# Optimization experiments

Hardware: AMD Instinct MI355X
Metric: run time of the kernel (lower is better)

The kernel has to match this reference:

```python
import jax, jax.numpy as jnp
import numpy as np

MIN_NORM = 1e-15
BALL_EPS = 4e-3  # float32 boundary eps used by the PoincareBall manifold


def _norm(x):
    return jnp.maximum(jnp.linalg.norm(x, axis=-1, keepdims=True), MIN_NORM)


def _artanh(x):
    # clamp like torch Artanh autograd fn (1e-7 margin)
    return jnp.arctanh(jnp.clip(x, -1.0 + 1e-7, 1.0 - 1e-7))


def proj(x, c):
    n = _norm(x)
    maxnorm = (1.0 - BALL_EPS) / jnp.sqrt(c)
    return jnp.where(n > maxnorm, x / n * maxnorm, x)


def expmap0(u, c):
    sc = jnp.sqrt(c)
    n = _norm(u)
    return jnp.tanh(sc * n) * u / (sc * n)


def logmap0(p, c):
    sc = jnp.sqrt(c)
    n = _norm(p)
    return _artanh(sc * n) * p / (sc * n)


def mobius_add(x, y, c):
    x2 = jnp.sum(x * x, axis=-1, keepdims=True)
    y2 = jnp.sum(y * y, axis=-1, keepdims=True)
    xy = jnp.sum(x * y, axis=-1, keepdims=True)
    num = (1.0 + 2.0 * c * xy + c * y2) * x + (1.0 - c * x2) * y
    denom = 1.0 + 2.0 * c * xy + c * c * x2 * y2
    return num / jnp.maximum(denom, MIN_NORM)


def mobius_matvec(m, x, c):
    sc = jnp.sqrt(c)
    xn = _norm(x)
    mx = x @ m.T  # [N, out]
    mxn = _norm(mx)
    res = jnp.tanh(mxn / xn * _artanh(sc * xn)) * mx / (mxn * sc)
    is_zero = jnp.all(mx == 0, axis=-1, keepdims=True)
    return jnp.where(is_zero, jnp.zeros_like(res), res)


def setup_inputs() -> dict:
    key = jax.random.key(0)
    N, D_IN, D_OUT, E = 100000, 128, 128, 1600000
    k1, k2, k3, k4, k5 = jax.random.split(key, 5)
    # points inside the Poincare ball (||x|| ~ 0.34 < 1)
    x = 0.03 * jax.random.normal(k1, (N, D_IN), dtype=jnp.float32)
    # xavier_uniform with gain sqrt(2)
    limit = np.sqrt(2.0) * np.sqrt(6.0 / (D_IN + D_OUT))
    weight = jax.random.uniform(k2, (D_OUT, D_IN), minval=-limit, maxval=limit, dtype=jnp.float32)
    bias = jnp.zeros((D_OUT,), dtype=jnp.float32)
    edge_index = jax.random.randint(k3, (2, E), 0, N, dtype=jnp.int64)
    edge_weight = jax.random.uniform(k4, (E,), dtype=jnp.float32) / 16.0
    return {"x": x, "weight": weight, "bias": bias,
            "edge_index": edge_index, "edge_weight": edge_weight,
            "num_nodes": N}


def reference(x, weight, bias, edge_index, edge_weight, num_nodes):
    c_in = 1.0
    c_out = 1.0
    # --- OriginHypLinear (dropout=0 / eval) ---
    mv = proj(mobius_matvec(weight, x, c_in), c_in)
    hyp_bias = proj(expmap0(bias[None, :], c_in), c_in)  # proj_tan0 is identity
    h = proj(mobius_add(mv, hyp_bias, c_in), c_in)
    # --- OriginHypAgg: logmap0 -> spmm -> expmap0 ---
    xt = logmap0(h, c_in)
    dst, src = edge_index[0], edge_index[1]
    support = jax.ops.segment_sum(edge_weight[:, None] * xt[src], dst,
                                  num_segments=num_nodes)
    h = proj(expmap0(support, c_in), c_in)
    # --- OriginHypAct: relu in tangent space ---
    xt = jax.nn.relu(logmap0(h, c_in))  # proj_tan0 identity
    return proj(expmap0(xt, c_out), c_out)
```

## Files before the change

kernel.cpp:

```cpp
#include <hip/hip_runtime.h>
#include <math.h>

#define D 128
#define MAXNORM 0.996f
#define MINNORM 1e-15f
#define ATCLAMP (1.0f - 1e-7f)

#define CHUNK 2048
#define BSH   7
#define MAXNB 1024
#define SCAP2 5120
#define CAP   4096
#define TCAP  (1 << 20)

typedef unsigned int   u32;
typedef unsigned short u16;

typedef __attribute__((ext_vector_type(8))) _Float16 f16x8;
typedef __attribute__((ext_vector_type(2))) __fp16   h2raw;
typedef __attribute__((ext_vector_type(4))) float f32x4;

__device__ __forceinline__ float wsum(float v) {
#pragma unroll
  for (int m = 32; m; m >>= 1) v += __shfl_xor(v, m);
  return v;
}
__device__ __forceinline__ float rsum16(float v) {
#pragma unroll
  for (int m = 1; m <= 8; m <<= 1) v += __shfl_xor(v, m);
  return v;
}

__device__ __forceinline__ float frcp(float x) { return __builtin_amdgcn_rcpf(x); }

__device__ __forceinline__ float fast_artanh(float x) {
  x = fminf(x, ATCLAMP);
  return 0.5f * __logf((1.0f + x) * frcp(1.0f - x));
}
__device__ __forceinline__ float fast_tanh(float z) {
  float t = __expf(-2.0f * z);
  return (1.0f - t) * frcp(1.0f + t);
}

__device__ __forceinline__ float bflo(u32 u) { return __uint_as_float(u << 16); }
__device__ __forceinline__ float bfhi(u32 u) { return __uint_as_float(u & 0xffff0000u); }
__device__ __forceinline__ float bf2f(u16 h) { return __uint_as_float(((u32)h) << 16); }

union H2U { h2raw h; u32 u; };
__device__ __forceinline__ u32 pkh(float a, float b) {
  H2U c; c.h = __builtin_amdgcn_cvt_pkrtz(a, b); return c.u;
}
union U2H { u32 u; _Float16 h[2]; };
union U4H8 { uint4 u; f16x8 h; };
__device__ __forceinline__ f16x8 as_h8(uint4 v) { U4H8 c; c.u = v; return c.h; }
__device__ __forceinline__ u16 f2h(float f) {
  _Float16 h = (_Float16)f; return *(u16*)&h;
}

__device__ __forceinline__ bool detect_bf16(const u32* p) {
  float lo = fabsf(bflo(p[threadIdx.x & 63]));
  return (bool)__all(lo < 1.0f);
}
__device__ __forceinline__ bool detect_i64(const int* p) {
  return (bool)__all(p[2 * (threadIdx.x & 63) + 1] == 0);
}

template<bool BF>
__device__ __forceinline__ void k1_body(const void* xv, const void* Wv,
                                        const void* bv, u16* xt, int N,
                                        uint4* Wh, int blk, int tbase) {
  const int tid  = threadIdx.x;
  const int lane = tid & 63;
  const int wid  = tid >> 6;
  const int qg   = lane >> 4;
  const int lc   = lane & 15;

  for (int slot = tid; slot < 2048; slot += 256) {
    const int l = slot & 63, frag = slot >> 6;
    const int t = frag >> 2, ks = frag & 3;
    const int j  = (l & 15) + 16 * t;
    const int k0 = 32 * ks + 8 * (l >> 4);
    float f[8];
    if (BF) {
      uint4 v = ((const uint4*)Wv)[j * 16 + (k0 >> 3)];
      f[0] = bflo(v.x); f[1] = bfhi(v.x); f[2] = bflo(v.y); f[3] = bfhi(v.y);
      f[4] = bflo(v.z); f[5] = bfhi(v.z); f[6] = bflo(v.w); f[7] = bfhi(v.w);
    } else {
      const float* Wf = (const float*)Wv;
      float4 f0 = *(const float4*)(Wf + (size_t)j * D + k0);
      float4 f1 = *(const float4*)(Wf + (size_t)j * D + k0 + 4);
      f[0]=f0.x; f[1]=f0.y; f[2]=f0.z; f[3]=f0.w;
      f[4]=f1.x; f[5]=f1.y; f[6]=f1.z; f[7]=f1.w;
    }
    Wh[slot] = make_uint4(pkh(f[0],f[1]), pkh(f[2],f[3]),
                          pkh(f[4],f[5]), pkh(f[6],f[7]));
  }

  float bfr[8];
  float nb2 = 0.f;
#pragma unroll
  for (int t = 0; t < 8; ++t) {
    float v = BF ? bf2f(((const u16*)bv)[lc + 16 * t])
                 : ((const float*)bv)[lc + 16 * t];
    bfr[t] = v; nb2 += v * v;
  }
  nb2 = rsum16(nb2);
  float y2;
  {
    float nb = fmaxf(sqrtf(nb2), MINNORM);
    float s  = fast_tanh(nb) * frcp(nb);
    float n1 = s * nb;
    if (n1 > MAXNORM) s *= MAXNORM * frcp(n1);
#pragma unroll
    for (int t = 0; t < 8; ++t) bfr[t] *= s;
    y2 = s * s * nb2;
  }
  const bool bias_zero = (y2 == 0.0f);

  __syncthreads();

  const int T = (N + 15) >> 4;
  const int tile = tbase + blk * 4 + wid;
  if (tile >= T) return;
  {
    const int rbase = tile * 16;
    int rowA = rbase + lc; if (rowA >= N) rowA = N - 1;
    uint4 Ah[4];
    float xn2 = 0.f;
#pragma unroll
    for (int ks = 0; ks < 4; ++ks) {
      float f[8];
      if (BF) {
        uint4 v = ((const uint4*)((const u16*)xv + (size_t)rowA * D))[4 * ks + qg];
        f[0]=bflo(v.x); f[1]=bfhi(v.x); f[2]=bflo(v.y); f[3]=bfhi(v.y);
        f[4]=bflo(v.z); f[5]=bfhi(v.z); f[6]=bflo(v.w); f[7]=bfhi(v.w);
      } else {
        const float4* xr = (const float4*)((const float*)xv + (size_t)rowA * D);
        float4 f0 = xr[8 * ks + 2 * qg], f1 = xr[8 * ks + 2 * qg + 1];
        f[0]=f0.x; f[1]=f0.y; f[2]=f0.z; f[3]=f0.w;
        f[4]=f1.x; f[5]=f1.y; f[6]=f1.z; f[7]=f1.w;
      }
#pragma unroll
      for (int i = 0; i < 8; ++i) xn2 += f[i] * f[i];
      Ah[ks] = make_uint4(pkh(f[0],f[1]), pkh(f[2],f[3]),
                          pkh(f[4],f[5]), pkh(f[6],f[7]));
    }
    xn2 += __shfl_xor(xn2, 16);
    xn2 += __shfl_xor(xn2, 32);

    f32x4 acc[8];
    const f32x4 zero = {0.f, 0.f, 0.f, 0.f};
#pragma unroll
    for (int t = 0; t < 8; ++t) acc[t] = zero;
#pragma unroll
    for (int ks = 0; ks < 4; ++ks) {
      f16x8 a = as_h8(Ah[ks]);
#pragma unroll
      for (int t = 0; t < 8; ++t) {
        f16x8 bh = as_h8(Wh[(t * 4 + ks) * 64 + lane]);
        acc[t] = __builtin_amdgcn_mfma_f32_16x16x32_f16(a, bh, acc[t], 0, 0, 0);
      }
    }

#pragma unroll
    for (int q = 0; q < 4; ++q) {
      const int row_off = qg * 4 + q;
      const int row = rbase + row_off;
      float xnq = fmaxf(sqrtf(__shfl(xn2, row_off)), MINNORM);
      float s2 = 0.f;
#pragma unroll
      for (int t = 0; t < 8; ++t) { float v = acc[t][q]; s2 += v * v; }
      s2 = rsum16(s2);
      float mxn = fmaxf(sqrtf(s2), MINNORM);
      float r = fast_tanh(mxn * frcp(xnq) * fast_artanh(xnq)) * frcp(mxn);
      float pn = r * mxn;
      if (pn > MAXNORM) { r *= MAXNORM * frcp(pn); pn = MAXNORM; }
      float h[8];
      float hn;
      if (bias_zero) {
#pragma unroll
        for (int t = 0; t < 8; ++t) h[t] = r * acc[t][q];
        hn = pn;
      } else {
        float xy = 0.f;
#pragma unroll
        for (int t = 0; t < 8; ++t) { h[t] = r * acc[t][q]; xy += h[t] * bfr[t]; }
        xy = rsum16(xy);
        float x2 = pn * pn;
        float ca = 1.f + 2.f * xy + y2;
        float cb = 1.f - x2;
        float id = frcp(fmaxf(1.f + 2.f * xy + x2 * y2, MINNORM));
        float s3 = 0.f;
#pragma unroll
        for (int t = 0; t < 8; ++t) { h[t] = (ca * h[t] + cb * bfr[t]) * id; s3 += h[t] * h[t]; }
        hn = fmaxf(sqrtf(rsum16(s3)), MINNORM);
      }
      float ps = (hn > MAXNORM) ? (MAXNORM * frcp(hn)) : 1.f;
      float np = fmaxf(hn * ps, MINNORM);
      float tsc = fast_artanh(np) * frcp(np) * ps;
      if (row < N) {
        uint4 pk;
        pk.x = (u32)f2h(tsc * h[0]) | ((u32)f2h(tsc * h[1]) << 16);
        pk.y = (u32)f2h(tsc * h[2]) | ((u32)f2h(tsc * h[3]) << 16);
        pk.z = (u32)f2h(tsc * h[4]) | ((u32)f2h(tsc * h[5]) << 16);
        pk.w = (u32)f2h(tsc * h[6]) | ((u32)f2h(tsc * h[7]) << 16);
        *(uint4*)(xt + (size_t)row * D + lc * 8) = pk;
      }
    }
  }
}

__device__ __forceinline__ void ksA_body(
    const int* ei, const void* ew, uint2* ebuck, u16* soffs,
    int E, int N, int nb, int chunk, uint4* lds) {
  uint2* recs = (uint2*)lds;
  int*   hist = (int*)(lds + 1024);
  int*   sArr = hist + MAXNB;
  int*   psum = sArr + MAXNB + 1;
  const bool i64 = detect_i64(ei);
  const bool bf  = detect_bf16((const u32*)ew);
  const int tid   = threadIdx.x;
  const int cbase = chunk * CHUNK;

  for (int i = tid; i < MAXNB; i += 256) hist[i] = 0;
  __syncthreads();

  int bkt[8], rank[8]; u32 px[8], wb[8]; bool val[8];
#pragma unroll
  for (int r = 0; r < 8; ++r) {
    const int e = cbase + r * 256 + tid;
    val[r] = false;
    if (e < E) {
      int dst, src;
      if (i64) {
        dst = (int)((const uint2*)ei)[(size_t)e].x;
        src = (int)((const uint2*)ei)[(size_t)E + e].x;
      } else {
        dst = ei[e]; src = ei[(size_t)E + e];
      }
      if ((unsigned)dst < (unsigned)N && (unsigned)src < (unsigned)N) {
        val[r] = true;
        bkt[r] = dst >> BSH;
        px[r]  = (u32)src | ((u32)(dst & ((1 << BSH) - 1)) << 17);
        float w;
        if (bf) w = bf2f(((const u16*)ew)[e]); else w = ((const float*)ew)[e];
        wb[r] = __float_as_uint(w);
        rank[r] = atomicAdd(&hist[bkt[r]], 1);
      }
    }
  }
  __syncthreads();

  const int g0 = tid * 4;
  int loc[4], ts = 0;
#pragma unroll
  for (int i = 0; i < 4; ++i) { loc[i] = ts; ts += hist[g0 + i]; }
  psum[tid] = ts; __syncthreads();
#pragma unroll
  for (int off = 1; off < 256; off <<= 1) {
    int t = (tid >= off) ? psum[tid - off] : 0;
    __syncthreads();
    psum[tid] += t;
    __syncthreads();
  }
  const int excl = psum[tid] - ts;
#pragma unroll
  for (int i = 0; i < 4; ++i) sArr[g0 + i] = excl + loc[i];
  if (tid == 255) sArr[MAXNB] = psum[255];
  __syncthreads();

#pragma unroll
  for (int r = 0; r < 8; ++r) if (val[r])
    recs[sArr[bkt[r]] + rank[r]] = make_uint2(px[r], wb[r]);
  __syncthreads();

  const int vcnt = sArr[MAXNB];
  for (int i = tid; i < vcnt; i += 256) ebuck[(size_t)cbase + i] = recs[i];
  u16* so = soffs + (size_t)chunk * (nb + 1);
  for (int b = tid; b <= nb; b += 256) so[b] = (u16)sArr[b];
}

extern "C" __global__ __launch_bounds__(256)
void OriginHyperbolicGraphConvolution_38628935860614_kernel(
    const void* x, const void* W, const void* b, u16* xt,
    const int* ei, const void* ew, uint2* ebuck, u16* soffs, int* tailcur,
    int N, int E, int nb, int nchunks) {
  __shared__ uint4 Wh[2048];
  if (blockIdx.x == 0 && threadIdx.x == 0) *tailcur = 0;
  if ((int)blockIdx.x < nchunks) {
    ksA_body(ei, ew, ebuck, soffs, E, N, nb, (int)blockIdx.x, Wh);
  } else {
    if (detect_bf16((const u32*)x))
      k1_body<true >(x, W, b, xt, N, Wh, (int)blockIdx.x - nchunks, 0);
    else
      k1_body<false>(x, W, b, xt, N, Wh, (int)blockIdx.x - nchunks, 0);
  }
}

__device__ __forceinline__ void ks3_body(
    const uint2* ebuck, const u16* soffs, uint2* esrt, uint2* offs2,
    int* tailcur, int N, int nb, int nchunks, int b, char* smem) {
  uint2* stage = (uint2*)smem;
  int*   red   = (int*)(smem + 40960);
  int*   hist  = (int*)(smem + 41984);
  int*   sc    = (int*)(smem + 42496);
  int*   cur   = (int*)(smem + 43008);
  int*   lcur  = (int*)(smem + 43520);
  u32*   sbase = (u32*)(smem + 43524);
  const int tid = threadIdx.x;
  const int node0 = b << BSH;

  int myc = 0;
  for (int c = tid; c < nchunks; c += 256) {
    const u16* so = soffs + (size_t)c * (nb + 1) + b;
    myc += (int)so[1] - (int)so[0];
  }
  red[tid] = myc;
  if (tid < 128) hist[tid] = 0;
  if (tid == 0) *lcur = 0;
  __syncthreads();
#pragma unroll
  for (int off = 128; off; off >>= 1) {
    if (tid < off) red[tid] += red[tid + off];
    __syncthreads();
  }
  const int cnt = red[0];
  if (tid == 0)
    *sbase = (cnt <= CAP) ? (u32)((size_t)b * CAP)
                          : (u32)((size_t)nb * CAP + (u32)atomicAdd(tailcur, cnt));
  __syncthreads();
  const u32 base = *sbase;

  const bool fit = (cnt <= SCAP2);
  if (fit) {
    for (int c = tid; c < nchunks; c += 256) {
      const u16* so = soffs + (size_t)c * (nb + 1) + b;
      const int a = so[0], e = so[1];
      if (e > a) {
        const int sb = atomicAdd(lcur, e - a);
        for (int j = a; j < e; ++j) {
          const uint2 r = ebuck[(size_t)c * CHUNK + j];
          stage[sb + (j - a)] = r;
          atomicAdd(&hist[(r.x >> 17) & 127], 1);
        }
      }
    }
  } else {
    for (int c = tid; c < nchunks; c += 256) {
      const u16* so = soffs + (size_t)c * (nb + 1) + b;
      for (int j = so[0]; j < so[1]; ++j)
        atomicAdd(&hist[(ebuck[(size_t)c * CHUNK + j].x >> 17) & 127], 1);
    }
  }
  __syncthreads();

  int v = 0;
  if (tid < 128) { v = hist[tid]; sc[tid] = v; }
  __syncthreads();
#pragma unroll
  for (int off = 1; off < 128; off <<= 1) {
    int t = (tid < 128 && tid >= off) ? sc[tid - off] : 0;
    __syncthreads();
    if (tid < 128) sc[tid] += t;
    __syncthreads();
  }
  if (tid < 128) {
    const int st = sc[tid] - v;
    cur[tid] = st;
    const int node = node0 + tid;
    if (node < N) offs2[node] = make_uint2(base + (u32)st, (u32)v);
  }
  __syncthreads();

  if (fit) {
    for (int i = tid; i < cnt; i += 256) {
      const uint2 r = stage[i];
      const int d = atomicAdd(&cur[(r.x >> 17) & 127], 1);
      esrt[(size_t)base + d] = make_uint2(r.x & 0x1FFFFu, r.y);
    }
  } else {
    for (int c = tid; c < nchunks; c += 256) {
      const u16* so = soffs + (size_t)c * (nb + 1) + b;
      for (int j = so[0]; j < so[1]; ++j) {
        const uint2 r = ebuck[(size_t)c * CHUNK + j];
        const int d = atomicAdd(&cur[(r.x >> 17) & 127], 1);
        esrt[(size_t)base + d] = make_uint2(r.x & 0x1FFFFu, r.y);
      }
    }
  }
}

extern "C" __global__ __launch_bounds__(256) void kB(
    const void* x, const void* W, const void* b, u16* xt,
    const uint2* ebuck, const u16* soffs, uint2* esrt, uint2* offs2,
    int* tailcur, int N, int nb, int nchunks, int tbase) {
  __shared__ uint4 smem[2721];
  if ((int)blockIdx.x < nb) {
    ks3_body(ebuck, soffs, esrt, offs2, tailcur, N, nb, nchunks,
             (int)blockIdx.x, (char*)smem);
  } else {
    if (detect_bf16((const u32*)x))
      k1_body<true >(x, W, b, xt, N, smem, (int)blockIdx.x - nb, tbase);
    else
      k1_body<false>(x, W, b, xt, N, smem, (int)blockIdx.x - nb, tbase);
  }
}

extern "C" __global__ __launch_bounds__(256) void kagg(
    const uint2* offs2, const uint2* esrt, const u16* xt,
    void* out, const void* xdet, int N) {
  const bool bf = detect_bf16((const u32*)xdet);
  const int lane = threadIdx.x & 63;
  const int node = blockIdx.x * 4 + (threadIdx.x >> 6);
  if (node >= N) return;
  const uint2 oo = offs2[node];
  const int s0  = __builtin_amdgcn_readfirstlane((int)oo.x);
  const int cnt = __builtin_amdgcn_readfirstlane((int)oo.y);
  const uint2* ep = esrt + s0;
  const u32* xtw = (const u32*)xt;
  float a0 = 0.f, a1 = 0.f;
  int i = 0;
  for (; i + 16 <= cnt; i += 16) {
    uint2 e[16]; u32 u[16];
#pragma unroll
    for (int k = 0; k < 16; ++k) e[k] = ep[i + k];
#pragma unroll
    for (int k = 0; k < 16; ++k) u[k] = xtw[(e[k].x << 6) | lane];
#pragma unroll
    for (int k = 0; k < 16; ++k) {
      const float w = __uint_as_float(e[k].y);
      U2H c; c.u = u[k];
      a0 += w * (float)c.h[0];
      a1 += w * (float)c.h[1];
    }
  }
  for (; i + 4 <= cnt; i += 4) {
    uint2 e[4]; u32 u[4];
#pragma unroll
    for (int k = 0; k < 4; ++k) e[k] = ep[i + k];
#pragma unroll
    for (int k = 0; k < 4; ++k) u[k] = xtw[(e[k].x << 6) | lane];
#pragma unroll
    for (int k = 0; k < 4; ++k) {
      const float w = __uint_as_float(e[k].y);
      U2H c; c.u = u[k];
      a0 += w * (float)c.h[0];
      a1 += w * (float)c.h[1];
    }
  }
  for (; i < cnt; ++i) {
    const uint2 e = ep[i];
    const u32 u = xtw[(e.x << 6) | lane];
    const float w = __uint_as_float(e.y);
    U2H c; c.u = u;
    a0 += w * (float)c.h[0];
    a1 += w * (float)c.h[1];
  }
  float n = fmaxf(sqrtf(wsum(a0 * a0 + a1 * a1)), MINNORM);
  float tn = fast_tanh(n);
  float m = tn * frcp(n);
  if (tn > MAXNORM) { m *= MAXNORM * frcp(tn); tn = MAXNORM; }
  float nn = fmaxf(tn, MINNORM);
  m *= fast_artanh(nn) * frcp(nn);
  float tA = fmaxf(m * a0, 0.f), tB = fmaxf(m * a1, 0.f);
  float nr = fmaxf(sqrtf(wsum(tA * tA + tB * tB)), MINNORM);
  float t2 = fast_tanh(nr);
  float m2 = t2 * frcp(nr);
  if (t2 > MAXNORM) m2 *= MAXNORM * frcp(t2);
  float oA = m2 * tA, oB = m2 * tB;
  const int ls = (lane & 7) * 8 + (lane >> 4);
  const int el = (lane >> 3) & 1;
  const float A0 = __shfl(oA, ls),     B0 = __shfl(oB, ls);
  const float A1 = __shfl(oA, ls + 4), B1 = __shfl(oB, ls + 4);
  const float v0 = el ? B0 : A0;
  const float v1 = el ? B1 : A1;
  if (bf) {
    u32 ua = __float_as_uint(v0), ub = __float_as_uint(v1);
    u32 ra = (ua + 0x7fffu + ((ua >> 16) & 1u)) >> 16;
    u32 rb = (ub + 0x7fffu + ((ub >> 16) & 1u)) >> 16;
    ((u32*)out)[(size_t)node * 64 + lane] = ra | (rb << 16);
  } else {
    ((float2*)out)[(size_t)node * 64 + lane] = make_float2(v0, v1);
  }
}

extern "C" void kernel_launch(void* const* d_in, const int* in_sizes, int n_in,
                              void* d_out, int out_size, void* d_ws, size_t ws_size,
                              hipStream_t stream) {
  const void* x    = d_in[0];
  const void* W    = d_in[1];
  const void* bias = d_in[2];
  const int*  ei   = (const int*)d_in[3];
  const void* ew   = d_in[4];
  const int N = in_sizes[0] / D;
  const int E = in_sizes[4];
  const int nchunks = (E + CHUNK - 1) / CHUNK;
  const int nb      = (N + (1 << BSH) - 1) >> BSH;

  char* ws = (char*)d_ws;
  size_t off = 0;
  auto carve = [&](size_t bytes) { char* p = ws + off; off = (off + bytes + 255) & ~(size_t)255; return p; };
  u16*   xt    = (u16*)  carve((size_t)N * D * sizeof(u16));
  uint2* ebuck = (uint2*)carve((size_t)nchunks * CHUNK * sizeof(uint2));
  uint2* esrt  = (uint2*)carve(((size_t)nb * CAP + TCAP) * sizeof(uint2));
  u16*   soffs = (u16*)  carve((size_t)nchunks * (nb + 1) * sizeof(u16));
  uint2* offs2 = (uint2*)carve((size_t)N * sizeof(uint2));
  int*   tailcur = (int*)carve(256);

  const int T    = (N + 15) / 16;
  const int nk1  = (T + 3) / 4;
  const int nk1a = nk1 / 2;
  const int nk1b = nk1 - nk1a;

  OriginHyperbolicGraphConvolution_38628935860614_kernel<<<nchunks + nk1a, 256, 0, stream>>>(
      x, W, bias, xt, ei, ew, ebuck, soffs, tailcur, N, E, nb, nchunks);
  kB<<<nb + nk1b, 256, 0, stream>>>(
      x, W, bias, xt, ebuck, soffs, esrt, offs2, tailcur, N, nb, nchunks, nk1a * 4);
  kagg<<<(N + 3) / 4, 256, 0, stream>>>(offs2, esrt, xt, d_out, x, N);
}
```

Before: 245.1 us.

## Scatter edge buckets directly to per-bucket slots via global atomic cursors

```diff
diff --git a/kernel.cpp b/kernel.cpp
--- a/kernel.cpp
+++ b/kernel.cpp
@@ -9,9 +9,11 @@
 #define CHUNK 2048
 #define BSH   7
 #define MAXNB 1024
-#define SCAP2 5120
-#define CAP   4096
-#define TCAP  (1 << 20)
+#define CAP   6144
+#define HALF  3072
+#define OCAP  131072
+#define TCAP  262144
+#define CURSTRIDE 16
 
 typedef unsigned int   u32;
 typedef unsigned short u16;
@@ -63,6 +65,11 @@
 }
 __device__ __forceinline__ bool detect_i64(const int* p) {
   return (bool)__all(p[2 * (threadIdx.x & 63) + 1] == 0);
+}
+
+extern "C" __global__ __launch_bounds__(256) void k0_zeroi(int* p, int n) {
+  int i = blockIdx.x * 256 + threadIdx.x;
+  if (i < n) p[i] = 0;
 }
 
 template<bool BF>
@@ -211,12 +218,14 @@
 }
 
 __device__ __forceinline__ void ksA_body(
-    const int* ei, const void* ew, uint2* ebuck, u16* soffs,
+    const int* ei, const void* ew, uint2* eslot, int* cursor,
+    uint2* ofl, int* oflb, int* oflcnt,
     int E, int N, int nb, int chunk, uint4* lds) {
   uint2* recs = (uint2*)lds;
-  int*   hist = (int*)(lds + 1024);
-  int*   sArr = hist + MAXNB;
-  int*   psum = sArr + MAXNB + 1;
+  int*   hist = (int*)((char*)lds + 16384);
+  int*   sArr = (int*)((char*)lds + 20480);
+  int*   psum = (int*)((char*)lds + 24580);
+  u16*   bof  = (u16*)((char*)lds + 25604);
   const bool i64 = detect_i64(ei);
   const bool bf  = detect_bf16((const u32*)ew);
   const int tid   = threadIdx.x;
@@ -270,25 +279,42 @@
   __syncthreads();
 
 #pragma unroll
-  for (int r = 0; r < 8; ++r) if (val[r])
-    recs[sArr[bkt[r]] + rank[r]] = make_uint2(px[r], wb[r]);
-  __syncthreads();
-
+  for (int r = 0; r < 8; ++r) if (val[r]) {
+    const int idx = sArr[bkt[r]] + rank[r];
+    recs[idx] = make_uint2(px[r], wb[r]);
+    bof[idx]  = (u16)bkt[r];
+  }
+  __syncthreads();
+
+  for (int b2 = tid; b2 < nb; b2 += 256) {
+    const int len = sArr[b2 + 1] - sArr[b2];
+    if (len > 0) hist[b2] = atomicAdd(&cursor[b2 * CURSTRIDE], len);
+  }
   const int vcnt = sArr[MAXNB];
-  for (int i = tid; i < vcnt; i += 256) ebuck[(size_t)cbase + i] = recs[i];
-  u16* so = soffs + (size_t)chunk * (nb + 1);
-  for (int b = tid; b <= nb; b += 256) so[b] = (u16)sArr[b];
+  __syncthreads();
+
+  for (int i = tid; i < vcnt; i += 256) {
+    const int bb = bof[i];
+    const int pos = hist[bb] + (i - sArr[bb]);
+    const uint2 r = recs[i];
+    if (pos < HALF) eslot[(size_t)bb * CAP + pos] = r;
+    else {
+      const int op = atomicAdd(oflcnt, 1);
+      if (op < OCAP) { ofl[op] = r; oflb[op] = bb; }
+    }
+  }
 }
 
 extern "C" __global__ __launch_bounds__(256)
 void OriginHyperbolicGraphConvolution_38628935860614_kernel(
     const void* x, const void* W, const void* b, u16* xt,
-    const int* ei, const void* ew, uint2* ebuck, u16* soffs, int* tailcur,
+    const int* ei, const void* ew, uint2* eslot, int* cursor,
+    uint2* ofl, int* oflb, int* oflcnt,
     int N, int E, int nb, int nchunks) {
   __shared__ uint4 Wh[2048];
-  if (blockIdx.x == 0 && threadIdx.x == 0) *tailcur = 0;
   if ((int)blockIdx.x < nchunks) {
-    ksA_body(ei, ew, ebuck, soffs, E, N, nb, (int)blockIdx.x, Wh);
+    ksA_body(ei, ew, eslot, cursor, ofl, oflb, oflcnt,
+             E, N, nb, (int)blockIdx.x, Wh);
   } else {
     if (detect_bf16((const u32*)x))
       k1_body<true >(x, W, b, xt, N, Wh, (int)blockIdx.x - nchunks, 0);
@@ -298,59 +324,24 @@
 }
 
 __device__ __forceinline__ void ks3_body(
-    const uint2* ebuck, const u16* soffs, uint2* esrt, uint2* offs2,
-    int* tailcur, int N, int nb, int nchunks, int b, char* smem) {
-  uint2* stage = (uint2*)smem;
-  int*   red   = (int*)(smem + 40960);
-  int*   hist  = (int*)(smem + 41984);
-  int*   sc    = (int*)(smem + 42496);
-  int*   cur   = (int*)(smem + 43008);
-  int*   lcur  = (int*)(smem + 43520);
-  u32*   sbase = (u32*)(smem + 43524);
+    uint2* eslot, const uint2* ofl, const int* oflb, const int* oflcnt,
+    const int* cursor, int* tailcur, uint2* offs2, int N, int nb, int b,
+    int* hist, int* sc, int* cur, int* smisc) {
   const int tid = threadIdx.x;
   const int node0 = b << BSH;
-
-  int myc = 0;
-  for (int c = tid; c < nchunks; c += 256) {
-    const u16* so = soffs + (size_t)c * (nb + 1) + b;
-    myc += (int)so[1] - (int)so[0];
-  }
-  red[tid] = myc;
+  const int cnt = cursor[b * CURSTRIDE];
+  const int inslot = min(cnt, HALF);
+  const uint2* seg = eslot + (size_t)b * CAP;
   if (tid < 128) hist[tid] = 0;
-  if (tid == 0) *lcur = 0;
-  __syncthreads();
-#pragma unroll
-  for (int off = 128; off; off >>= 1) {
-    if (tid < off) red[tid] += red[tid + off];
-    __syncthreads();
-  }
-  const int cnt = red[0];
-  if (tid == 0)
-    *sbase = (cnt <= CAP) ? (u32)((size_t)b * CAP)
-                          : (u32)((size_t)nb * CAP + (u32)atomicAdd(tailcur, cnt));
-  __syncthreads();
-  const u32 base = *sbase;
-
-  const bool fit = (cnt <= SCAP2);
-  if (fit) {
-    for (int c = tid; c < nchunks; c += 256) {
-      const u16* so = soffs + (size_t)c * (nb + 1) + b;
-      const int a = so[0], e = so[1];
-      if (e > a) {
-        const int sb = atomicAdd(lcur, e - a);
-        for (int j = a; j < e; ++j) {
-          const uint2 r = ebuck[(size_t)c * CHUNK + j];
-          stage[sb + (j - a)] = r;
-          atomicAdd(&hist[(r.x >> 17) & 127], 1);
-        }
-      }
-    }
-  } else {
-    for (int c = tid; c < nchunks; c += 256) {
-      const u16* so = soffs + (size_t)c * (nb + 1) + b;
-      for (int j = so[0]; j < so[1]; ++j)
-        atomicAdd(&hist[(ebuck[(size_t)c * CHUNK + j].x >> 17) & 127], 1);
-    }
+  __syncthreads();
+
+  for (int i = tid; i < inslot; i += 256)
+    atomicAdd(&hist[(seg[i].x >> 17) & 127], 1);
+  int nof = 0;
+  if (cnt > HALF) {
+    nof = min(*oflcnt, OCAP);
+    for (int i = tid; i < nof; i += 256)
+      if (oflb[i] == b) atomicAdd(&hist[(ofl[i].x >> 17) & 127], 1);
   }
   __syncthreads();
 
@@ -364,6 +355,11 @@
     if (tid < 128) sc[tid] += t;
     __syncthreads();
   }
+  if (tid == 0)
+    smisc[0] = (cnt <= HALF) ? (int)((size_t)b * CAP + HALF)
+                             : (int)((size_t)nb * CAP + atomicAdd(tailcur, cnt));
+  __syncthreads();
+  const u32 base = (u32)smisc[0];
   if (tid < 128) {
     const int st = sc[tid] - v;
     cur[tid] = st;
@@ -372,32 +368,33 @@
   }
   __syncthreads();
 
-  if (fit) {
-    for (int i = tid; i < cnt; i += 256) {
-      const uint2 r = stage[i];
+  for (int i = tid; i < inslot; i += 256) {
+    const uint2 r = seg[i];
+    const int d = atomicAdd(&cur[(r.x >> 17) & 127], 1);
+    eslot[(size_t)base + d] = make_uint2(r.x & 0x1FFFFu, r.y);
+  }
+  if (cnt > HALF) {
+    for (int i = tid; i < nof; i += 256) if (oflb[i] == b) {
+      const uint2 r = ofl[i];
       const int d = atomicAdd(&cur[(r.x >> 17) & 127], 1);
-      esrt[(size_t)base + d] = make_uint2(r.x & 0x1FFFFu, r.y);
-    }
-  } else {
-    for (int c = tid; c < nchunks; c += 256) {
-      const u16* so = soffs + (size_t)c * (nb + 1) + b;
-      for (int j = so[0]; j < so[1]; ++j) {
-        const uint2 r = ebuck[(size_t)c * CHUNK + j];
-        const int d = atomicAdd(&cur[(r.x >> 17) & 127], 1);
-        esrt[(size_t)base + d] = make_uint2(r.x & 0x1FFFFu, r.y);
-      }
+      eslot[(size_t)base + d] = make_uint2(r.x & 0x1FFFFu, r.y);
     }
   }
 }
 
 extern "C" __global__ __launch_bounds__(256) void kB(
     const void* x, const void* W, const void* b, u16* xt,
-    const uint2* ebuck, const u16* soffs, uint2* esrt, uint2* offs2,
-    int* tailcur, int N, int nb, int nchunks, int tbase) {
-  __shared__ uint4 smem[2721];
+    uint2* eslot, const uint2* ofl, const int* oflb, const int* oflcnt,
+    const int* cursor, int* tailcur, uint2* offs2,
+    int N, int nb, int tbase) {
+  __shared__ uint4 smem[2048];
   if ((int)blockIdx.x < nb) {
-    ks3_body(ebuck, soffs, esrt, offs2, tailcur, N, nb, nchunks,
-             (int)blockIdx.x, (char*)smem);
+    int* hist  = (int*)smem;
+    int* sc    = hist + 128;
+    int* cur   = sc + 128;
+    int* smisc = cur + 128;
+    ks3_body(eslot, ofl, oflb, oflcnt, cursor, tailcur, offs2,
+             N, nb, (int)blockIdx.x, hist, sc, cur, smisc);
   } else {
     if (detect_bf16((const u32*)x))
       k1_body<true >(x, W, b, xt, N, smem, (int)blockIdx.x - nb, tbase);
@@ -407,7 +404,7 @@
 }
 
 extern "C" __global__ __launch_bounds__(256) void kagg(
-    const uint2* offs2, const uint2* esrt, const u16* xt,
+    const uint2* offs2, const uint2* eslot, const u16* xt,
     void* out, const void* xdet, int N) {
   const bool bf = detect_bf16((const u32*)xdet);
   const int lane = threadIdx.x & 63;
@@ -416,7 +413,7 @@
   const uint2 oo = offs2[node];
   const int s0  = __builtin_amdgcn_readfirstlane((int)oo.x);
   const int cnt = __builtin_amdgcn_readfirstlane((int)oo.y);
-  const uint2* ep = esrt + s0;
+  const uint2* ep = eslot + s0;
   const u32* xtw = (const u32*)xt;
   float a0 = 0.f, a1 = 0.f;
   int i = 0;
@@ -501,20 +498,26 @@
   size_t off = 0;
   auto carve = [&](size_t bytes) { char* p = ws + off; off = (off + bytes + 255) & ~(size_t)255; return p; };
   u16*   xt    = (u16*)  carve((size_t)N * D * sizeof(u16));
-  uint2* ebuck = (uint2*)carve((size_t)nchunks * CHUNK * sizeof(uint2));
-  uint2* esrt  = (uint2*)carve(((size_t)nb * CAP + TCAP) * sizeof(uint2));
-  u16*   soffs = (u16*)  carve((size_t)nchunks * (nb + 1) * sizeof(u16));
+  uint2* eslot = (uint2*)carve(((size_t)nb * CAP + TCAP) * sizeof(uint2));
+  uint2* ofl   = (uint2*)carve((size_t)OCAP * sizeof(uint2));
+  int*   oflb  = (int*)  carve((size_t)OCAP * sizeof(int));
   uint2* offs2 = (uint2*)carve((size_t)N * sizeof(uint2));
-  int*   tailcur = (int*)carve(256);
-
+  int*   czone = (int*)  carve(((size_t)nb * CURSTRIDE + 2) * sizeof(int));
+  int*   cursor  = czone;
+  int*   oflcnt  = czone + (size_t)nb * CURSTRIDE;
+  int*   tailcur = oflcnt + 1;
+
+  const int nz   = nb * CURSTRIDE + 2;
   const int T    = (N + 15) / 16;
   const int nk1  = (T + 3) / 4;
   const int nk1a = nk1 / 2;
-  const int nk1b = nk1 - nk1a;
-
+  const int tA   = nk1a * 4;
+  const int nk1b = (T - tA + 3) / 4;
+
+  k0_zeroi<<<(nz + 255) / 256, 256, 0, stream>>>(czone, nz);
   OriginHyperbolicGraphConvolution_38628935860614_kernel<<<nchunks + nk1a, 256, 0, stream>>>(
-      x, W, bias, xt, ei, ew, ebuck, soffs, tailcur, N, E, nb, nchunks);
+      x, W, bias, xt, ei, ew, eslot, cursor, ofl, oflb, oflcnt, N, E, nb, nchunks);
   kB<<<nb + nk1b, 256, 0, stream>>>(
-      x, W, bias, xt, ebuck, soffs, esrt, offs2, tailcur, N, nb, nchunks, nk1a * 4);
-  kagg<<<(N + 3) / 4, 256, 0, stream>>>(offs2, esrt, xt, d_out, x, N);
-}
+      x, W, bias, xt, eslot, ofl, oflb, oflcnt, cursor, tailcur, offs2, N, nb, tA);
+  kagg<<<(N + 3) / 4, 256, 0, stream>>>(offs2, eslot, xt, d_out, x, N);
+}
```

Result: slower. 263.9 us (+7.7%).
